# Kernel optimization log

Measured on AMD Instinct MI355X. Metric: run time of the kernel, lower is better.

The kernel has to match this reference:

```python
import jax, jax.numpy as jnp
import numpy as np

NEG_SLOPE_MLP = 0.1   # F.leaky_relu(x, 0.1) used throughout the repo
NEG_SLOPE_GAT = 0.2   # PyG GATv2Conv default negative_slope
HEADS = 2
OUT = 8


def lrelu(x):
    return jax.nn.leaky_relu(x, NEG_SLOPE_MLP)


def gatv2_conv(x, src, dst, e_attr, wl, bl, wr, br, we, att, bias):
    """PyG-style GATv2Conv with edge features, concat heads.
    x: [N, Din], src/dst: [E], e_attr: [E, 2]
    wl/wr: [heads*out, Din], we: [heads*out, 2], att: [heads, out], bias: [heads*out]
    """
    N = x.shape[0]
    xl = (x @ wl.T + bl).reshape(N, HEADS, OUT)   # source transform
    xr = (x @ wr.T + br).reshape(N, HEADS, OUT)   # target transform
    e = (e_attr @ we.T).reshape(-1, HEADS, OUT)
    m = jax.nn.leaky_relu(xl[src] + xr[dst] + e, NEG_SLOPE_GAT)   # [E, H, O]
    logits = jnp.einsum('ehd,hd->eh', m, att)                      # [E, H]
    # numerically-stable segment softmax over incoming edges of each dst node
    mx = jax.ops.segment_max(logits, dst, num_segments=N)          # [N, H]
    a = jnp.exp(logits - mx[dst])
    denom = jax.ops.segment_sum(a, dst, num_segments=N)
    alpha = a / (denom[dst] + 1e-16)                               # [E, H]
    out = jax.ops.segment_sum(xl[src] * alpha[..., None], dst, num_segments=N)
    return out.reshape(N, HEADS * OUT) + bias                      # [N, 16]


def setup_inputs() -> dict:
    key = jax.random.key(0)
    ks = iter(jax.random.split(key, 64))
    N, E = 250000, 5000000
    inp = {
        'x': jax.random.normal(next(ks), (N, 3), jnp.float32),
        'edge_index': jax.random.randint(next(ks), (2, E), 0, N, jnp.int32),
        'edge_attr': jax.random.normal(next(ks), (E, 2), jnp.float32),
        'meta_data': jax.random.normal(next(ks), (6,), jnp.float32),
    }
    shapes = dict(
        ft1_w=(8, 3), ft1_b=(8,), ft2_w=(8, 8), ft2_b=(8,),
        g1_wl=(16, 8), g1_bl=(16,), g1_wr=(16, 8), g1_br=(16,), g1_we=(16, 2), g1_att=(2, 8), g1_bias=(16,),
        g2_wl=(16, 16), g2_bl=(16,), g2_wr=(16, 16), g2_br=(16,), g2_we=(16, 2), g2_att=(2, 8), g2_bias=(16,),
        sp1_w=(64, 16), sp1_b=(64,), sp2_w=(16, 64), sp2_b=(16,),
        me_w=(8, 6), me_b=(8,),
        fc1_w=(24, 24), fc1_b=(24,), fc2_w=(8, 24), fc2_b=(8,), fc3_w=(3, 8), fc3_b=(3,),
    )
    for name, shp in shapes.items():
        inp[name] = 0.2 * jax.random.normal(next(ks), shp, jnp.float32)
    return inp


def reference(x, edge_index, edge_attr, meta_data,
              ft1_w, ft1_b, ft2_w, ft2_b,
              g1_wl, g1_bl, g1_wr, g1_br, g1_we, g1_att, g1_bias,
              g2_wl, g2_bl, g2_wr, g2_br, g2_we, g2_att, g2_bias,
              sp1_w, sp1_b, sp2_w, sp2_b, me_w, me_b,
              fc1_w, fc1_b, fc2_w, fc2_b, fc3_w, fc3_b):
    src, dst = edge_index[0], edge_index[1]
    # tiny per-node MLP feature transform
    h = lrelu(x @ ft1_w.T + ft1_b)
    h = lrelu(h @ ft2_w.T + ft2_b)                              # [N, 8]
    # 2-layer GATv2 block (activation between layers)
    h = gatv2_conv(h, src, dst, edge_attr, g1_wl, g1_bl, g1_wr, g1_br, g1_we, g1_att, g1_bias)
    h = lrelu(h)
    h = gatv2_conv(h, src, dst, edge_attr, g2_wl, g2_bl, g2_wr, g2_br, g2_we, g2_att, g2_bias)  # [N, 16]
    # sum pool over all nodes + small MLP
    p = h.sum(axis=0)                                           # [16]
    p = lrelu(p @ sp1_w.T + sp1_b)
    p = p @ sp2_w.T + sp2_b                                     # [16]
    # meta data encoder
    m = lrelu(meta_data @ me_w.T + me_b)                        # [8]
    z = jnp.concatenate([p, m], axis=0)                         # [24]
    z = lrelu(z @ fc1_w.T + fc1_b)
    z = lrelu(z @ fc2_w.T + fc2_b)
    # dropout is identity in eval/reference mode
    z = z @ fc3_w.T + fc3_b                                     # [3]
    return jax.nn.softmax(z[None, :], axis=1)                   # [1, 3]
```

## Files before the change

kernel.cpp:

```cpp
#include <hip/hip_runtime.h>
#include <hip/hip_bf16.h>
#include <hip/hip_fp16.h>
#include <math.h>


#define HO 16
#define BSHIFT 8
#define BNODES 256
#define PT 512
#define PCHUNK 6144
#define CAP2 6016

typedef __attribute__((ext_vector_type(2))) float v2f;

__device__ __forceinline__ float lrelu(float x, float s) { return x > 0.f ? x : s * x; }

__device__ __forceinline__ uint2 pack_fp8x8(const float* v) {
    int a = __builtin_amdgcn_cvt_pk_fp8_f32(v[0], v[1], 0, false);
    a     = __builtin_amdgcn_cvt_pk_fp8_f32(v[2], v[3], a, true);
    int b = __builtin_amdgcn_cvt_pk_fp8_f32(v[4], v[5], 0, false);
    b     = __builtin_amdgcn_cvt_pk_fp8_f32(v[6], v[7], b, true);
    return make_uint2((unsigned int)a, (unsigned int)b);
}

__device__ __forceinline__ void unpack_fp8x8(uint2 u, float* v) {
    v2f f0 = __builtin_amdgcn_cvt_pk_f32_fp8((int)u.x, false);
    v2f f1 = __builtin_amdgcn_cvt_pk_f32_fp8((int)u.x, true);
    v2f f2 = __builtin_amdgcn_cvt_pk_f32_fp8((int)u.y, false);
    v2f f3 = __builtin_amdgcn_cvt_pk_f32_fp8((int)u.y, true);
    v[0]=f0.x; v[1]=f0.y; v[2]=f1.x; v[3]=f1.y;
    v[4]=f2.x; v[5]=f2.y; v[6]=f3.x; v[7]=f3.y;
}

__global__ void __launch_bounds__(256) node_l1(
    const float* __restrict__ x,
    const float* __restrict__ ft1_w, const float* __restrict__ ft1_b,
    const float* __restrict__ ft2_w, const float* __restrict__ ft2_b,
    const float* __restrict__ wl, const float* __restrict__ bl,
    const float* __restrict__ wr, const float* __restrict__ br,
    uint2* __restrict__ xlA, float* __restrict__ xr, int N)
{
    int n = blockIdx.x * 256 + threadIdx.x;
    if (n >= N) return;
    float x0 = x[3*n], x1 = x[3*n+1], x2 = x[3*n+2];
    float h1[8];
#pragma unroll
    for (int j = 0; j < 8; j++) {
        float a = ft1_w[3*j]*x0 + ft1_w[3*j+1]*x1 + ft1_w[3*j+2]*x2 + ft1_b[j];
        h1[j] = lrelu(a, 0.1f);
    }
    float h2[8];
#pragma unroll
    for (int j = 0; j < 8; j++) {
        float a = ft2_b[j];
#pragma unroll
        for (int k = 0; k < 8; k++) a += ft2_w[8*j+k]*h1[k];
        h2[j] = lrelu(a, 0.1f);
    }
    float ol[HO], orr[HO];
#pragma unroll
    for (int j = 0; j < HO; j++) {
        float a = bl[j], b = br[j];
#pragma unroll
        for (int k = 0; k < 8; k++) { a += wl[8*j+k]*h2[k]; b += wr[8*j+k]*h2[k]; }
        ol[j] = a; orr[j] = b;
    }
    uint2 p0 = pack_fp8x8(ol);
    uint2 p1 = pack_fp8x8(ol + 8);
    ((uint4*)xlA)[n] = make_uint4(p0.x, p0.y, p1.x, p1.y);
    float4* xr4 = (float4*)(xr + (size_t)n*HO);
#pragma unroll
    for (int q = 0; q < 4; q++)
        xr4[q] = make_float4(orr[4*q], orr[4*q+1], orr[4*q+2], orr[4*q+3]);
}

__global__ void __launch_bounds__(256) k_binit(int* __restrict__ bcur)
{
    int b = blockIdx.x * 256 + threadIdx.x;
    if (b < 1024) bcur[b] = b * CAP2;
}

__global__ void __launch_bounds__(PT) k_part(
    const int* __restrict__ src, const int* __restrict__ dst,
    const float* __restrict__ eattr, int* __restrict__ bcur,
    uint2* __restrict__ grecs, int E)
{
    __shared__ int hist[1024], lofs[1024], gofs[1024], lcur[1024];
    __shared__ int scan_s[PT];
    __shared__ uint2 srecs[PCHUNK];
    __shared__ unsigned short bid[PCHUNK];
    int t = threadIdx.x;
    int base = blockIdx.x * PCHUNK;
    int cnt = E - base; if (cnt > PCHUNK) cnt = PCHUNK;

    for (int b = t; b < 1024; b += PT) hist[b] = 0;
    __syncthreads();
    for (int i = t; i < cnt; i += PT)
        atomicAdd(&hist[dst[base + i] >> BSHIFT], 1);
    __syncthreads();
    int h0 = hist[2*t], h1 = hist[2*t+1];
    int pair = h0 + h1;
    scan_s[t] = pair;
    __syncthreads();
    for (int off = 1; off < PT; off <<= 1) {
        int add = (t >= off) ? scan_s[t - off] : 0;
        __syncthreads();
        scan_s[t] += add;
        __syncthreads();
    }
    int pbase = scan_s[t] - pair;
    lofs[2*t]   = pbase;
    lofs[2*t+1] = pbase + h0;
    __syncthreads();
    for (int b = t; b < 1024; b += PT) {
        int c = hist[b];
        int g = (c > 0) ? atomicAdd(&bcur[b], c) : 0;
        gofs[b] = g - lofs[b];
        lcur[b] = 0;
    }
    __syncthreads();
    for (int i = t; i < cnt; i += PT) {
        int e = base + i;
        int d = dst[e];
        int b = d >> BSHIFT;
        float2 ea = ((const float2*)eattr)[e];
        __half2 hv = __floats2half2_rn(ea.x, ea.y);
        unsigned int eb = *reinterpret_cast<unsigned int*>(&hv);
        int q = atomicAdd(&lcur[b], 1);
        int idx = lofs[b] + q;
        srecs[idx] = make_uint2(((unsigned int)src[e] << 8) | (unsigned int)(d & (BNODES-1)), eb);
        bid[idx] = (unsigned short)b;
    }
    __syncthreads();
    for (int i = t; i < cnt; i += PT) {
        int b = bid[i];
        int pos = gofs[b] + i;
        if (pos < (b + 1) * CAP2) grecs[pos] = srecs[i];
    }
}

__global__ void __launch_bounds__(256) k_fine(
    const int* __restrict__ bcur, uint2* recs,
    int* __restrict__ rowS, int* __restrict__ rowE, int N)
{
    __shared__ uint2 rout[CAP2];
    __shared__ int lhist[256], lsc[256], lcur2[256];
    int b = blockIdx.x;
    int bstart = b * CAP2;
    int cnt = bcur[b] - bstart;
    if (cnt > CAP2) cnt = CAP2;
    if (cnt < 0) cnt = 0;
    int t = threadIdx.x;
    lhist[t] = 0;
    __syncthreads();
    for (int i = t; i < cnt; i += 256)
        atomicAdd(&lhist[recs[bstart + i].x & (BNODES-1)], 1);
    __syncthreads();
    int v = lhist[t];
    lsc[t] = v;
    __syncthreads();
    for (int off = 1; off < 256; off <<= 1) {
        int add = (t >= off) ? lsc[t - off] : 0;
        __syncthreads();
        lsc[t] += add;
        __syncthreads();
    }
    int ex = lsc[t] - v;
    lcur2[t] = ex;
    int n = (b << BSHIFT) + t;
    if (n < N) { rowS[n] = bstart + ex; rowE[n] = bstart + ex + v; }
    __syncthreads();
    for (int i = t; i < cnt; i += 256) {
        uint2 r = recs[bstart + i];
        int p = atomicAdd(&lcur2[r.x & (BNODES-1)], 1);
        rout[p] = make_uint2(r.x >> 8, r.y);
    }
    __syncthreads();
    for (int i = t; i < cnt; i += 256)
        recs[bstart + i] = rout[i];
}

struct AggState { float m, s, acc[8]; };

__device__ __forceinline__ void agg_edge(
    AggState& st, const float* va, const float* xd,
    const float* w0, const float* w1, const float* at,
    float ea0, float ea1)
{
    float lg = 0.f;
#pragma unroll
    for (int o = 0; o < 8; o++) {
        float mv = va[o] + xd[o] + (w0[o]*ea0 + w1[o]*ea1);
        mv = mv > 0.f ? mv : 0.2f*mv;
        lg += mv * at[o];
    }
    float nm = fmaxf(st.m, lg);
    float sc = __expf(st.m - nm);
    float wv = __expf(lg - nm);
    st.s = st.s*sc + wv;
#pragma unroll
    for (int o = 0; o < 8; o++) st.acc[o] = st.acc[o]*sc + wv*va[o];
    st.m = nm;
}

__device__ __forceinline__ void agg_one(
    AggState& st, uint2 r, uint2 g, const float* xd,
    const float* w0, const float* w1, const float* at)
{
    float v[8];
    unpack_fp8x8(g, v);
    __half2 h2 = *reinterpret_cast<__half2*>(&r.y);
    agg_edge(st, v, xd, w0, w1, at, __low2float(h2), __high2float(h2));
}

__device__ __forceinline__ void agg_row(
    int rs, int re, int hu,
    const uint2* __restrict__ recs, const uint2* __restrict__ xl8,
    const float* xd, const float* w0, const float* w1, const float* at,
    AggState& st)
{
    st.m = -INFINITY; st.s = 0.f;
#pragma unroll
    for (int o = 0; o < 8; o++) st.acc[o] = 0.f;
    int i = rs;
    for (; i + 4 <= re; i += 4) {
        uint2 r0 = recs[i], r1 = recs[i+1], r2 = recs[i+2], r3 = recs[i+3];
        uint2 g0 = xl8[(size_t)r0.x*2 + hu];
        uint2 g1 = xl8[(size_t)r1.x*2 + hu];
        uint2 g2 = xl8[(size_t)r2.x*2 + hu];
        uint2 g3 = xl8[(size_t)r3.x*2 + hu];
        agg_one(st, r0, g0, xd, w0, w1, at);
        agg_one(st, r1, g1, xd, w0, w1, at);
        agg_one(st, r2, g2, xd, w0, w1, at);
        agg_one(st, r3, g3, xd, w0, w1, at);
    }
    for (; i < re; i++) {
        uint2 r0 = recs[i];
        uint2 g0 = xl8[(size_t)r0.x*2 + hu];
        agg_one(st, r0, g0, xd, w0, w1, at);
    }
}

__global__ void __launch_bounds__(256, 4) node_agg_l1(
    const int* __restrict__ rowS, const int* __restrict__ rowE,
    const uint2* __restrict__ recs,
    const uint2* __restrict__ xlA, float* xr,
    const float* __restrict__ we, const float* __restrict__ att,
    const float* __restrict__ bias,
    const float* __restrict__ wl2, const float* __restrict__ bl2,
    const float* __restrict__ wr2, const float* __restrict__ br2,
    uint2* __restrict__ xlB, int N)
{
    __shared__ float sh[256][8];
    int t = threadIdx.x;
    int hu = __builtin_amdgcn_readfirstlane(t >> 7);
    int n = blockIdx.x * 128 + (t & 127);
    bool alive = (n < N);
    int kb = hu * 8;
    float w0[8], w1[8], at[8];
#pragma unroll
    for (int o = 0; o < 8; o++) {
        w0[o] = we[2*(kb+o)];
        w1[o] = we[2*(kb+o)+1];
        at[o] = att[kb+o];
    }
    float xd[8];
    {
        size_t nn = alive ? (size_t)n : 0;
        const float4* xrp = (const float4*)(xr + nn*HO + kb);
        float4 d0 = xrp[0], d1 = xrp[1];
        xd[0]=d0.x; xd[1]=d0.y; xd[2]=d0.z; xd[3]=d0.w;
        xd[4]=d1.x; xd[5]=d1.y; xd[6]=d1.z; xd[7]=d1.w;
    }
    int rs = alive ? rowS[n] : 0;
    int re = alive ? rowE[n] : 0;
    AggState st;
    agg_row(rs, re, hu, recs, xlA, xd, w0, w1, at, st);

    float inv = 1.f/(st.s + 1e-16f);
    float hh[8];
#pragma unroll
    for (int o = 0; o < 8; o++) hh[o] = lrelu(st.acc[o]*inv + bias[kb+o], 0.1f);
#pragma unroll
    for (int o = 0; o < 8; o++) sh[t][o] = hh[o];
    __syncthreads();
    if (!alive) return;
    int partner = t ^ 128;
    float h0v[8], h1v[8];
#pragma unroll
    for (int o = 0; o < 8; o++) {
        float oth = sh[partner][o];
        h0v[o] = hu ? oth : hh[o];
        h1v[o] = hu ? hh[o] : oth;
    }
    float ol[8], orr[8];
#pragma unroll
    for (int jo = 0; jo < 8; jo++) {
        int j = kb + jo;
        float a = bl2[j], b = br2[j];
#pragma unroll
        for (int k = 0; k < 8; k++) { a += wl2[HO*j+k]*h0v[k];   b += wr2[HO*j+k]*h0v[k]; }
#pragma unroll
        for (int k = 0; k < 8; k++) { a += wl2[HO*j+8+k]*h1v[k]; b += wr2[HO*j+8+k]*h1v[k]; }
        ol[jo] = a; orr[jo] = b;
    }
    xlB[(size_t)n*2 + hu] = pack_fp8x8(ol);
    float4* xr4 = (float4*)(xr + (size_t)n*HO + kb);
    xr4[0] = make_float4(orr[0], orr[1], orr[2], orr[3]);
    xr4[1] = make_float4(orr[4], orr[5], orr[6], orr[7]);
}

__global__ void __launch_bounds__(256, 4) node_agg_l2(
    const int* __restrict__ rowS, const int* __restrict__ rowE,
    const uint2* __restrict__ recs,
    const uint2* __restrict__ xlB, const float* __restrict__ xr,
    const float* __restrict__ we, const float* __restrict__ att,
    const float* __restrict__ bias, float* __restrict__ partials, int pstride, int N)
{
    int t = threadIdx.x;
    int hu = __builtin_amdgcn_readfirstlane(t >> 7);
    int n = blockIdx.x * 128 + (t & 127);
    bool alive = (n < N);
    int kb = hu * 8;
    float w0[8], w1[8], at[8];
#pragma unroll
    for (int o = 0; o < 8; o++) {
        w0[o] = we[2*(kb+o)];
        w1[o] = we[2*(kb+o)+1];
        at[o] = att[kb+o];
    }
    float xd[8];
    {
        size_t nn = alive ? (size_t)n : 0;
        const float4* xrp = (const float4*)(xr + nn*HO + kb);
        float4 d0 = xrp[0], d1 = xrp[1];
        xd[0]=d0.x; xd[1]=d0.y; xd[2]=d0.z; xd[3]=d0.w;
        xd[4]=d1.x; xd[5]=d1.y; xd[6]=d1.z; xd[7]=d1.w;
    }
    int rs = alive ? rowS[n] : 0;
    int re = alive ? rowE[n] : 0;
    AggState st;
    agg_row(rs, re, hu, recs, xlB, xd, w0, w1, at, st);

    float out[8];
    if (alive) {
        float inv = 1.f/(st.s + 1e-16f);
#pragma unroll
        for (int o = 0; o < 8; o++) out[o] = st.acc[o]*inv + bias[kb+o];
    } else {
#pragma unroll
        for (int o = 0; o < 8; o++) out[o] = 0.f;
    }
#pragma unroll
    for (int off = 32; off >= 1; off >>= 1) {
#pragma unroll
        for (int o = 0; o < 8; o++) out[o] += __shfl_down(out[o], off, 64);
    }
    __shared__ float sm[4][8];
    int wave = t >> 6, lane = t & 63;
    if (lane == 0) {
#pragma unroll
        for (int o = 0; o < 8; o++) sm[wave][o] = out[o];
    }
    __syncthreads();
    if (t < 16) {
        int hp = t >> 3, oo = t & 7;
        float tt = sm[2*hp][oo] + sm[2*hp+1][oo];
        partials[(size_t)(hp*8 + oo) * pstride + blockIdx.x] = tt;
    }
}

__global__ void __launch_bounds__(256) k_reduce(
    const float* __restrict__ partials, int pstride, int nparts,
    float* __restrict__ pool)
{
    __shared__ float s[256];
    int c = blockIdx.x;
    int t = threadIdx.x;
    const float* col = partials + (size_t)c * pstride;
    float acc = 0.f;
    for (int r = t; r < nparts; r += 256) acc += col[r];
    s[t] = acc;
    __syncthreads();
#pragma unroll
    for (int off = 128; off > 0; off >>= 1) {
        if (t < off) s[t] += s[t + off];
        __syncthreads();
    }
    if (t == 0) pool[c] = s[0];
}

__global__ void __launch_bounds__(64) final_mlp(
    const float* __restrict__ pool, const float* __restrict__ meta,
    const float* __restrict__ sp1_w, const float* __restrict__ sp1_b,
    const float* __restrict__ sp2_w, const float* __restrict__ sp2_b,
    const float* __restrict__ me_w, const float* __restrict__ me_b,
    const float* __restrict__ fc1_w, const float* __restrict__ fc1_b,
    const float* __restrict__ fc2_w, const float* __restrict__ fc2_b,
    const float* __restrict__ fc3_w, const float* __restrict__ fc3_b,
    float* __restrict__ out)
{
    __shared__ float s1[64], zb[24], z1[24], z2[8];
    int t = threadIdx.x;
    {
        float acc = sp1_b[t];
        for (int k = 0; k < 16; k++) acc += pool[k]*sp1_w[t*16+k];
        s1[t] = lrelu(acc, 0.1f);
    }
    __syncthreads();
    if (t < 16) {
        float acc = sp2_b[t];
        for (int k = 0; k < 64; k++) acc += s1[k]*sp2_w[t*64+k];
        zb[t] = acc;
    } else if (t < 24) {
        int j = t - 16;
        float acc = me_b[j];
        for (int k = 0; k < 6; k++) acc += meta[k]*me_w[j*6+k];
        zb[t] = lrelu(acc, 0.1f);
    }
    __syncthreads();
    if (t < 24) {
        float acc = fc1_b[t];
        for (int k = 0; k < 24; k++) acc += zb[k]*fc1_w[t*24+k];
        z1[t] = lrelu(acc, 0.1f);
    }
    __syncthreads();
    if (t < 8) {
        float acc = fc2_b[t];
        for (int k = 0; k < 24; k++) acc += z1[k]*fc2_w[t*24+k];
        z2[t] = lrelu(acc, 0.1f);
    }
    __syncthreads();
    if (t == 0) {
        float z3[3]; float mxv = -1e30f;
        for (int j = 0; j < 3; j++) {
            float acc = fc3_b[j];
            for (int k = 0; k < 8; k++) acc += z2[k]*fc3_w[j*8+k];
            z3[j] = acc; mxv = fmaxf(mxv, acc);
        }
        float s = 0.f;
        for (int j = 0; j < 3; j++) { z3[j] = __expf(z3[j]-mxv); s += z3[j]; }
        for (int j = 0; j < 3; j++) out[j] = z3[j]/s;
    }
}

extern "C" void kernel_launch(void* const* d_in, const int* in_sizes, int n_in,
                              void* d_out, int out_size, void* d_ws, size_t ws_size,
                              hipStream_t stream)
{
    const float* x      = (const float*)d_in[0];
    const int*   eidx   = (const int*)  d_in[1];
    const float* eattr  = (const float*)d_in[2];
    const float* meta   = (const float*)d_in[3];
    const float* ft1_w  = (const float*)d_in[4];
    const float* ft1_b  = (const float*)d_in[5];
    const float* ft2_w  = (const float*)d_in[6];
    const float* ft2_b  = (const float*)d_in[7];
    const float* g1_wl  = (const float*)d_in[8];
    const float* g1_bl  = (const float*)d_in[9];
    const float* g1_wr  = (const float*)d_in[10];
    const float* g1_br  = (const float*)d_in[11];
    const float* g1_we  = (const float*)d_in[12];
    const float* g1_att = (const float*)d_in[13];
    const float* g1_bias= (const float*)d_in[14];
    const float* g2_wl  = (const float*)d_in[15];
    const float* g2_bl  = (const float*)d_in[16];
    const float* g2_wr  = (const float*)d_in[17];
    const float* g2_br  = (const float*)d_in[18];
    const float* g2_we  = (const float*)d_in[19];
    const float* g2_att = (const float*)d_in[20];
    const float* g2_bias= (const float*)d_in[21];
    const float* sp1_w  = (const float*)d_in[22];
    const float* sp1_b  = (const float*)d_in[23];
    const float* sp2_w  = (const float*)d_in[24];
    const float* sp2_b  = (const float*)d_in[25];
    const float* me_w   = (const float*)d_in[26];
    const float* me_b   = (const float*)d_in[27];
    const float* fc1_w  = (const float*)d_in[28];
    const float* fc1_b  = (const float*)d_in[29];
    const float* fc2_w  = (const float*)d_in[30];
    const float* fc2_b  = (const float*)d_in[31];
    const float* fc3_w  = (const float*)d_in[32];
    const float* fc3_b  = (const float*)d_in[33];
    float* out = (float*)d_out;

    const int N = in_sizes[0] / 3;
    const int E = in_sizes[2] / 2;
    const int* src = eidx;
    const int* dst = eidx + E;

    const int BN    = (N + 255) / 256;
    const int BN2   = (2*N + 255) / 256;
    const int NBUCK = (N + BNODES - 1) >> BSHIFT;
    const int BP    = (E + PCHUNK - 1) / PCHUNK;
    const int pstride = (BN2 + 63) & ~63;

    char* w = (char*)d_ws;
    size_t off = 0;
    auto take = [&](size_t bytes) { size_t o = off; off += (bytes + 255) & ~(size_t)255; return o; };
    int*    rowS     = (int*)   (w + take((size_t)4*N));
    int*    rowE     = (int*)   (w + take((size_t)4*N));
    int*    bcur     = (int*)   (w + take(4096));
    float*  pool     = (float*) (w + take(64));
    float*  partials = (float*) (w + take((size_t)4*16*pstride));
    uint2*  recs     = (uint2*) (w + take((size_t)8*NBUCK*CAP2));
    uint2*  xlA      = (uint2*) (w + take((size_t)16*N));
    uint2*  xlB      = (uint2*) (w + take((size_t)16*N));
    float*  xr       = (float*) (w + take((size_t)64*N));

    node_l1<<<BN, 256, 0, stream>>>(x, ft1_w, ft1_b, ft2_w, ft2_b,
                                    g1_wl, g1_bl, g1_wr, g1_br, xlA, xr, N);
    k_binit<<<4, 256, 0, stream>>>(bcur);
    k_part<<<BP, PT, 0, stream>>>(src, dst, eattr, bcur, recs, E);
    k_fine<<<NBUCK, 256, 0, stream>>>(bcur, recs, rowS, rowE, N);

    node_agg_l1<<<BN2, 256, 0, stream>>>(rowS, rowE, recs, xlA, xr,
                                         g1_we, g1_att, g1_bias,
                                         g2_wl, g2_bl, g2_wr, g2_br, xlB, N);
    node_agg_l2<<<BN2, 256, 0, stream>>>(rowS, rowE, recs, xlB, xr,
                                         g2_we, g2_att, g2_bias, partials, pstride, N);
    k_reduce<<<16, 256, 0, stream>>>(partials, pstride, BN2, pool);
    final_mlp<<<1, 64, 0, stream>>>(pool, meta, sp1_w, sp1_b, sp2_w, sp2_b,
                                    me_w, me_b, fc1_w, fc1_b, fc2_w, fc2_b,
                                    fc3_w, fc3_b, out);
}
```

Before: 448.4 us.

## Vectorize edge aggregation math to packed float2 and use wave-shuffle scans

The per-edge GATv2 logit and online-softmax accumulation now run on 2-wide float vectors, so the compiler can emit packed FP32 instructions (v_pk_fma/v_pk_mul) and the fp8 unpack feeds those vectors directly. The block-wide prefix scans in the partition and fine-sort kernels are replaced by wave-level shuffle scans plus a tiny cross-wave fixup, removing many syncthreads barriers. Leaky ReLU is computed as max(x, 0.2x), which is equivalent for a positive slope. The packed math depends on the compiler actually emitting packed ops, and the reduction order of the logit changes slightly.

After: 438.6 us. 1.02x faster.

```diff
diff --git a/kernel.cpp b/kernel.cpp
--- a/kernel.cpp
+++ b/kernel.cpp
@@ -23,13 +23,11 @@
     return make_uint2((unsigned int)a, (unsigned int)b);
 }
 
-__device__ __forceinline__ void unpack_fp8x8(uint2 u, float* v) {
-    v2f f0 = __builtin_amdgcn_cvt_pk_f32_fp8((int)u.x, false);
-    v2f f1 = __builtin_amdgcn_cvt_pk_f32_fp8((int)u.x, true);
-    v2f f2 = __builtin_amdgcn_cvt_pk_f32_fp8((int)u.y, false);
-    v2f f3 = __builtin_amdgcn_cvt_pk_f32_fp8((int)u.y, true);
-    v[0]=f0.x; v[1]=f0.y; v[2]=f1.x; v[3]=f1.y;
-    v[4]=f2.x; v[5]=f2.y; v[6]=f3.x; v[7]=f3.y;
+__device__ __forceinline__ void unpack_fp8x8v(uint2 u, v2f* v) {
+    v[0] = __builtin_amdgcn_cvt_pk_f32_fp8((int)u.x, false);
+    v[1] = __builtin_amdgcn_cvt_pk_f32_fp8((int)u.x, true);
+    v[2] = __builtin_amdgcn_cvt_pk_f32_fp8((int)u.y, false);
+    v[3] = __builtin_amdgcn_cvt_pk_f32_fp8((int)u.y, true);
 }
 
 __global__ void __launch_bounds__(256) node_l1(
@@ -86,7 +84,7 @@
     uint2* __restrict__ grecs, int E)
 {
     __shared__ int hist[1024], lofs[1024], gofs[1024], lcur[1024];
-    __shared__ int scan_s[PT];
+    __shared__ int wsum[8];
     __shared__ uint2 srecs[PCHUNK];
     __shared__ unsigned short bid[PCHUNK];
     int t = threadIdx.x;
@@ -100,15 +98,22 @@
     __syncthreads();
     int h0 = hist[2*t], h1 = hist[2*t+1];
     int pair = h0 + h1;
-    scan_s[t] = pair;
-    __syncthreads();
-    for (int off = 1; off < PT; off <<= 1) {
-        int add = (t >= off) ? scan_s[t - off] : 0;
-        __syncthreads();
-        scan_s[t] += add;
-        __syncthreads();
-    }
-    int pbase = scan_s[t] - pair;
+    int lane = t & 63;
+    int v = pair;
+#pragma unroll
+    for (int off = 1; off < 64; off <<= 1) {
+        int u = __shfl_up(v, off, 64);
+        if (lane >= off) v += u;
+    }
+    if (lane == 63) wsum[t >> 6] = v;
+    __syncthreads();
+    if (t == 0) {
+        int run = 0;
+#pragma unroll
+        for (int w8 = 0; w8 < 8; w8++) { int xv = wsum[w8]; wsum[w8] = run; run += xv; }
+    }
+    __syncthreads();
+    int pbase = v + wsum[t >> 6] - pair;
     lofs[2*t]   = pbase;
     lofs[2*t+1] = pbase + h0;
     __syncthreads();
@@ -144,7 +149,8 @@
     int* __restrict__ rowS, int* __restrict__ rowE, int N)
 {
     __shared__ uint2 rout[CAP2];
-    __shared__ int lhist[256], lsc[256], lcur2[256];
+    __shared__ int lhist[256], lcur2[256];
+    __shared__ int wsum[4];
     int b = blockIdx.x;
     int bstart = b * CAP2;
     int cnt = bcur[b] - bstart;
@@ -157,15 +163,22 @@
         atomicAdd(&lhist[recs[bstart + i].x & (BNODES-1)], 1);
     __syncthreads();
     int v = lhist[t];
-    lsc[t] = v;
-    __syncthreads();
-    for (int off = 1; off < 256; off <<= 1) {
-        int add = (t >= off) ? lsc[t - off] : 0;
-        __syncthreads();
-        lsc[t] += add;
-        __syncthreads();
-    }
-    int ex = lsc[t] - v;
+    int lane = t & 63;
+    int sv = v;
+#pragma unroll
+    for (int off = 1; off < 64; off <<= 1) {
+        int u = __shfl_up(sv, off, 64);
+        if (lane >= off) sv += u;
+    }
+    if (lane == 63) wsum[t >> 6] = sv;
+    __syncthreads();
+    if (t == 0) {
+        int run = 0;
+#pragma unroll
+        for (int w4 = 0; w4 < 4; w4++) { int xv = wsum[w4]; wsum[w4] = run; run += xv; }
+    }
+    __syncthreads();
+    int ex = sv + wsum[t >> 6] - v;
     lcur2[t] = ex;
     int n = (b << BSHIFT) + t;
     if (n < N) { rowS[n] = bstart + ex; rowE[n] = bstart + ex + v; }
@@ -180,35 +193,36 @@
         recs[bstart + i] = rout[i];
 }
 
-struct AggState { float m, s, acc[8]; };
+struct AggState { float m, s; v2f acc[4]; };
 
 __device__ __forceinline__ void agg_edge(
-    AggState& st, const float* va, const float* xd,
-    const float* w0, const float* w1, const float* at,
+    AggState& st, const v2f* va, const v2f* xd,
+    const v2f* w0, const v2f* w1, const v2f* at,
     float ea0, float ea1)
 {
-    float lg = 0.f;
-#pragma unroll
-    for (int o = 0; o < 8; o++) {
-        float mv = va[o] + xd[o] + (w0[o]*ea0 + w1[o]*ea1);
-        mv = mv > 0.f ? mv : 0.2f*mv;
-        lg += mv * at[o];
-    }
+    v2f lg2 = {0.f, 0.f};
+#pragma unroll
+    for (int q = 0; q < 4; q++) {
+        v2f mv = va[q] + xd[q] + w0[q]*ea0 + w1[q]*ea1;
+        mv = __builtin_elementwise_max(mv, mv * 0.2f);
+        lg2 = lg2 + mv*at[q];
+    }
+    float lg = lg2.x + lg2.y;
     float nm = fmaxf(st.m, lg);
     float sc = __expf(st.m - nm);
     float wv = __expf(lg - nm);
     st.s = st.s*sc + wv;
 #pragma unroll
-    for (int o = 0; o < 8; o++) st.acc[o] = st.acc[o]*sc + wv*va[o];
+    for (int q = 0; q < 4; q++) st.acc[q] = st.acc[q]*sc + va[q]*wv;
     st.m = nm;
 }
 
 __device__ __forceinline__ void agg_one(
-    AggState& st, uint2 r, uint2 g, const float* xd,
-    const float* w0, const float* w1, const float* at)
-{
-    float v[8];
-    unpack_fp8x8(g, v);
+    AggState& st, uint2 r, uint2 g, const v2f* xd,
+    const v2f* w0, const v2f* w1, const v2f* at)
+{
+    v2f v[4];
+    unpack_fp8x8v(g, v);
     __half2 h2 = *reinterpret_cast<__half2*>(&r.y);
     agg_edge(st, v, xd, w0, w1, at, __low2float(h2), __high2float(h2));
 }
@@ -216,12 +230,12 @@
 __device__ __forceinline__ void agg_row(
     int rs, int re, int hu,
     const uint2* __restrict__ recs, const uint2* __restrict__ xl8,
-    const float* xd, const float* w0, const float* w1, const float* at,
+    const v2f* xd, const v2f* w0, const v2f* w1, const v2f* at,
     AggState& st)
 {
     st.m = -INFINITY; st.s = 0.f;
 #pragma unroll
-    for (int o = 0; o < 8; o++) st.acc[o] = 0.f;
+    for (int q = 0; q < 4; q++) st.acc[q] = (v2f){0.f, 0.f};
     int i = rs;
     for (; i + 4 <= re; i += 4) {
         uint2 r0 = recs[i], r1 = recs[i+1], r2 = recs[i+2], r3 = recs[i+3];
@@ -257,20 +271,21 @@
     int n = blockIdx.x * 128 + (t & 127);
     bool alive = (n < N);
     int kb = hu * 8;
-    float w0[8], w1[8], at[8];
-#pragma unroll
-    for (int o = 0; o < 8; o++) {
-        w0[o] = we[2*(kb+o)];
-        w1[o] = we[2*(kb+o)+1];
-        at[o] = att[kb+o];
-    }
-    float xd[8];
+    v2f w0[4], w1[4], at[4];
+#pragma unroll
+    for (int q = 0; q < 4; q++) {
+        int o = kb + 2*q;
+        w0[q] = (v2f){we[2*o],   we[2*(o+1)]};
+        w1[q] = (v2f){we[2*o+1], we[2*(o+1)+1]};
+        at[q] = (v2f){att[o],    att[o+1]};
+    }
+    v2f xd[4];
     {
         size_t nn = alive ? (size_t)n : 0;
         const float4* xrp = (const float4*)(xr + nn*HO + kb);
         float4 d0 = xrp[0], d1 = xrp[1];
-        xd[0]=d0.x; xd[1]=d0.y; xd[2]=d0.z; xd[3]=d0.w;
-        xd[4]=d1.x; xd[5]=d1.y; xd[6]=d1.z; xd[7]=d1.w;
+        xd[0] = (v2f){d0.x, d0.y}; xd[1] = (v2f){d0.z, d0.w};
+        xd[2] = (v2f){d1.x, d1.y}; xd[3] = (v2f){d1.z, d1.w};
     }
     int rs = alive ? rowS[n] : 0;
     int re = alive ? rowE[n] : 0;
@@ -278,9 +293,11 @@
     agg_row(rs, re, hu, recs, xlA, xd, w0, w1, at, st);
 
     float inv = 1.f/(st.s + 1e-16f);
+    float accs[8] = {st.acc[0].x, st.acc[0].y, st.acc[1].x, st.acc[1].y,
+                     st.acc[2].x, st.acc[2].y, st.acc[3].x, st.acc[3].y};
     float hh[8];
 #pragma unroll
-    for (int o = 0; o < 8; o++) hh[o] = lrelu(st.acc[o]*inv + bias[kb+o], 0.1f);
+    for (int o = 0; o < 8; o++) hh[o] = lrelu(accs[o]*inv + bias[kb+o], 0.1f);
 #pragma unroll
     for (int o = 0; o < 8; o++) sh[t][o] = hh[o];
     __syncthreads();
@@ -322,20 +339,21 @@
     int n = blockIdx.x * 128 + (t & 127);
     bool alive = (n < N);
     int kb = hu * 8;
-    float w0[8], w1[8], at[8];
-#pragma unroll
-    for (int o = 0; o < 8; o++) {
-        w0[o] = we[2*(kb+o)];
-        w1[o] = we[2*(kb+o)+1];
-        at[o] = att[kb+o];
-    }
-    float xd[8];
+    v2f w0[4], w1[4], at[4];
+#pragma unroll
+    for (int q = 0; q < 4; q++) {
+        int o = kb + 2*q;
+        w0[q] = (v2f){we[2*o],   we[2*(o+1)]};
+        w1[q] = (v2f){we[2*o+1], we[2*(o+1)+1]};
+        at[q] = (v2f){att[o],    att[o+1]};
+    }
+    v2f xd[4];
     {
         size_t nn = alive ? (size_t)n : 0;
         const float4* xrp = (const float4*)(xr + nn*HO + kb);
         float4 d0 = xrp[0], d1 = xrp[1];
-        xd[0]=d0.x; xd[1]=d0.y; xd[2]=d0.z; xd[3]=d0.w;
-        xd[4]=d1.x; xd[5]=d1.y; xd[6]=d1.z; xd[7]=d1.w;
+        xd[0] = (v2f){d0.x, d0.y}; xd[1] = (v2f){d0.z, d0.w};
+        xd[2] = (v2f){d1.x, d1.y}; xd[3] = (v2f){d1.z, d1.w};
     }
     int rs = alive ? rowS[n] : 0;
     int re = alive ? rowE[n] : 0;
@@ -345,8 +363,10 @@
     float out[8];
     if (alive) {
         float inv = 1.f/(st.s + 1e-16f);
-#pragma unroll
-        for (int o = 0; o < 8; o++) out[o] = st.acc[o]*inv + bias[kb+o];
+        float accs[8] = {st.acc[0].x, st.acc[0].y, st.acc[1].x, st.acc[1].y,
+                         st.acc[2].x, st.acc[2].y, st.acc[3].x, st.acc[3].y};
+#pragma unroll
+        for (int o = 0; o < 8; o++) out[o] = accs[o]*inv + bias[kb+o];
     } else {
 #pragma unroll
         for (int o = 0; o < 8; o++) out[o] = 0.f;
```
